# Kernel optimization log

Hardware: AMD Instinct MI355X
Metric: run time of the kernel (lower is better)

The kernel has to match this reference:

```python
import jax, jax.numpy as jnp
import numpy as np

NUM_USERS = 1_000_000
NUM_ITEMS = 1_000_000
NUM_UFEAT = 100_000
NUM_IFEAT = 100_000
DIM = 64
BATCH = 16384
T_U = 327_680   # total flat user-feature tokens (~20/sample)
T_I = 819_200   # total flat item-feature tokens (~50/sample)


def setup_inputs() -> dict:
    key = jax.random.key(0)
    ks = jax.random.split(key, 12)
    inp = {
        "user_ids": jax.random.randint(ks[0], (BATCH,), 0, NUM_USERS),
        "item_ids": jax.random.randint(ks[1], (BATCH,), 0, NUM_ITEMS),
        "user_feat_idx": jax.random.randint(ks[2], (T_U,), 0, NUM_UFEAT),
        "user_feat_val": jax.random.uniform(ks[3], (T_U,), dtype=jnp.float32),
        "user_seg": jnp.sort(jax.random.randint(ks[4], (T_U,), 0, BATCH)),
        "item_feat_idx": jax.random.randint(ks[5], (T_I,), 0, NUM_IFEAT),
        "item_feat_val": jax.random.uniform(ks[6], (T_I,), dtype=jnp.float32),
        "item_seg": jnp.sort(jax.random.randint(ks[7], (T_I,), 0, BATCH)),
        # parameters (xavier-normal-style scale)
        "user_emb": jax.random.normal(ks[8], (NUM_USERS, DIM), jnp.float32) * 0.02,
        "item_emb": jax.random.normal(ks[9], (NUM_ITEMS, DIM), jnp.float32) * 0.02,
        "user_feat_emb": jax.random.normal(ks[10], (NUM_UFEAT, DIM), jnp.float32) * 0.02,
        "item_feat_emb": jax.random.normal(ks[11], (NUM_IFEAT, DIM), jnp.float32) * 0.02,
        "user_bias": jnp.zeros((NUM_USERS,), jnp.float32),
        "item_bias": jnp.zeros((NUM_ITEMS,), jnp.float32),
        "global_bias": jnp.zeros((), jnp.float32),
    }
    return inp


def _ragged_weighted_sum(table, idx, val, seg):
    # gather rows [T, D], weight, segment-reduce to [BATCH, D]
    rows = table[idx] * val[:, None]
    return jax.ops.segment_sum(rows, seg, num_segments=BATCH)


def reference(user_ids, item_ids, user_feat_idx, user_feat_val, user_seg,
              item_feat_idx, item_feat_val, item_seg,
              user_emb, item_emb, user_feat_emb, item_feat_emb,
              user_bias, item_bias, global_bias):
    u_feat = _ragged_weighted_sum(user_feat_emb, user_feat_idx, user_feat_val, user_seg)
    i_feat = _ragged_weighted_sum(item_feat_emb, item_feat_idx, item_feat_val, item_seg)
    u = user_emb[user_ids] + u_feat          # [B, D]
    v = item_emb[item_ids] + i_feat          # [B, D]
    pred = jnp.sum(u * v, axis=1)
    pred = pred + user_bias[user_ids] + item_bias[item_ids] + global_bias
    return pred
```

## Files before the change

### kernel.cpp

```cpp
#include <hip/hip_runtime.h>

#define DIM 64

static __device__ __forceinline__ int lower_bound(const int* __restrict__ a, int n, int v) {
    int lo = 0, hi = n;
    while (lo < hi) {
        int m = (lo + hi) >> 1;
        if (a[m] < v) lo = m + 1; else hi = m;
    }
    return lo;
}

__global__ __launch_bounds__(256) void mf_fwd_kernel(
    const int* __restrict__ user_ids, const int* __restrict__ item_ids,
    const int* __restrict__ u_idx, const float* __restrict__ u_val,
    const int* __restrict__ u_seg,
    const int* __restrict__ i_idx, const float* __restrict__ i_val,
    const int* __restrict__ i_seg,
    const float* __restrict__ user_emb, const float* __restrict__ item_emb,
    const float* __restrict__ ufeat_emb, const float* __restrict__ ifeat_emb,
    const float* __restrict__ user_bias, const float* __restrict__ item_bias,
    const float* __restrict__ global_bias,
    float* __restrict__ out,
    int batch, int Tu, int Ti)
{
    const int lane = threadIdx.x & 63;
    const int wave = threadIdx.x >> 6;
    const int b = (blockIdx.x << 2) + wave;
    if (b >= batch) return;

    int us  = __builtin_amdgcn_readfirstlane(lower_bound(u_seg, Tu, b));
    int ue  = __builtin_amdgcn_readfirstlane(lower_bound(u_seg, Tu, b + 1));
    int is0 = __builtin_amdgcn_readfirstlane(lower_bound(i_seg, Ti, b));
    int ie  = __builtin_amdgcn_readfirstlane(lower_bound(i_seg, Ti, b + 1));

    const int uid = user_ids[b];
    const int iid = item_ids[b];

    float u = user_emb[(size_t)uid * DIM + lane];
    for (int t = us; t < ue; ++t) {
        int   r = u_idx[t];
        float w = u_val[t];
        u = fmaf(ufeat_emb[(size_t)r * DIM + lane], w, u);
    }

    float v = item_emb[(size_t)iid * DIM + lane];
    for (int t = is0; t < ie; ++t) {
        int   r = i_idx[t];
        float w = i_val[t];
        v = fmaf(ifeat_emb[(size_t)r * DIM + lane], w, v);
    }

    float p = u * v;
    #pragma unroll
    for (int off = 32; off > 0; off >>= 1)
        p += __shfl_xor(p, off, 64);

    if (lane == 0)
        out[b] = p + user_bias[uid] + item_bias[iid] + global_bias[0];
}

extern "C" void kernel_launch(void* const* d_in, const int* in_sizes, int n_in,
                              void* d_out, int out_size, void* d_ws, size_t ws_size,
                              hipStream_t stream) {
    const int*   user_ids    = (const int*)d_in[0];
    const int*   item_ids    = (const int*)d_in[1];
    const int*   u_idx       = (const int*)d_in[2];
    const float* u_val       = (const float*)d_in[3];
    const int*   u_seg       = (const int*)d_in[4];
    const int*   i_idx       = (const int*)d_in[5];
    const float* i_val       = (const float*)d_in[6];
    const int*   i_seg       = (const int*)d_in[7];
    const float* user_emb    = (const float*)d_in[8];
    const float* item_emb    = (const float*)d_in[9];
    const float* ufeat_emb   = (const float*)d_in[10];
    const float* ifeat_emb   = (const float*)d_in[11];
    const float* user_bias   = (const float*)d_in[12];
    const float* item_bias   = (const float*)d_in[13];
    const float* global_bias = (const float*)d_in[14];
    float* out = (float*)d_out;

    const int batch = in_sizes[0];
    const int Tu    = in_sizes[2];
    const int Ti    = in_sizes[5];

    const int blocks = (batch + 3) / 4;
    mf_fwd_kernel<<<blocks, 256, 0, stream>>>(
        user_ids, item_ids, u_idx, u_val, u_seg, i_idx, i_val, i_seg,
        user_emb, item_emb, ufeat_emb, ifeat_emb, user_bias, item_bias,
        global_bias, out, batch, Tu, Ti);
}
```

Measured before the change: 574.0 us.

## Split wave into four token groups with float4 row loads and unrolled gathers

Each 64-lane wave is split into four 16-lane groups. Each group reads a full 64-float row with float4 loads and handles every fourth token, with the token loop unrolled by eight so many independent gathers are in flight. Partial sums are combined across groups with xor shuffles, and the dot product is reduced within 16 lanes. This targets the latency-bound serial per-token gather loop, at the cost of extra masked loads on the tail iterations and more shuffle work.

```diff
diff --git a/kernel.cpp b/kernel.cpp
--- a/kernel.cpp
+++ b/kernel.cpp
@@ -1,6 +1,7 @@
 #include <hip/hip_runtime.h>
 
 #define DIM 64
+#define UNR 8
 
 static __device__ __forceinline__ int lower_bound(const int* __restrict__ a, int n, int v) {
     int lo = 0, hi = n;
@@ -9,6 +10,43 @@
         if (a[m] < v) lo = m + 1; else hi = m;
     }
     return lo;
+}
+
+static __device__ __forceinline__ float4 ragged_accum4(
+    const float* __restrict__ table,
+    const int* __restrict__ idx, const float* __restrict__ val,
+    int ts, int te, int g, int l)
+{
+    float4 acc = {0.f, 0.f, 0.f, 0.f};
+    const int n = te - ts;
+    if (n <= 0) return acc;
+    const int iters = (n + 4 * UNR - 1) / (4 * UNR);
+    for (int it = 0; it < iters; ++it) {
+        const int base = ts + it * 4 * UNR + g;
+        #pragma unroll
+        for (int j = 0; j < UNR; ++j) {
+            int tt  = base + 4 * j;
+            int ttc = min(tt, te - 1);
+            int   r = idx[ttc];
+            float w = (tt < te) ? val[ttc] : 0.0f;
+            const float4 row = *(const float4*)(table + (size_t)r * DIM + 4 * l);
+            acc.x = fmaf(row.x, w, acc.x);
+            acc.y = fmaf(row.y, w, acc.y);
+            acc.z = fmaf(row.z, w, acc.z);
+            acc.w = fmaf(row.w, w, acc.w);
+        }
+    }
+    return acc;
+}
+
+static __device__ __forceinline__ void group_reduce4(float4& a) {
+    #pragma unroll
+    for (int off = 16; off < 64; off <<= 1) {
+        a.x += __shfl_xor(a.x, off, 64);
+        a.y += __shfl_xor(a.y, off, 64);
+        a.z += __shfl_xor(a.z, off, 64);
+        a.w += __shfl_xor(a.w, off, 64);
+    }
 }
 
 __global__ __launch_bounds__(256) void mf_fwd_kernel(
@@ -26,6 +64,8 @@
 {
     const int lane = threadIdx.x & 63;
     const int wave = threadIdx.x >> 6;
+    const int g = lane >> 4;
+    const int l = lane & 15;
     const int b = (blockIdx.x << 2) + wave;
     if (b >= batch) return;
 
@@ -37,23 +77,21 @@
     const int uid = user_ids[b];
     const int iid = item_ids[b];
 
-    float u = user_emb[(size_t)uid * DIM + lane];
-    for (int t = us; t < ue; ++t) {
-        int   r = u_idx[t];
-        float w = u_val[t];
-        u = fmaf(ufeat_emb[(size_t)r * DIM + lane], w, u);
-    }
+    const float4 u0 = *(const float4*)(user_emb + (size_t)uid * DIM + 4 * l);
+    const float4 v0 = *(const float4*)(item_emb + (size_t)iid * DIM + 4 * l);
 
-    float v = item_emb[(size_t)iid * DIM + lane];
-    for (int t = is0; t < ie; ++t) {
-        int   r = i_idx[t];
-        float w = i_val[t];
-        v = fmaf(ifeat_emb[(size_t)r * DIM + lane], w, v);
-    }
+    float4 ua = ragged_accum4(ufeat_emb, u_idx, u_val, us,  ue, g, l);
+    float4 va = ragged_accum4(ifeat_emb, i_idx, i_val, is0, ie, g, l);
 
-    float p = u * v;
+    group_reduce4(ua);
+    group_reduce4(va);
+
+    const float ux = ua.x + u0.x, uy = ua.y + u0.y, uz = ua.z + u0.z, uw = ua.w + u0.w;
+    const float vx = va.x + v0.x, vy = va.y + v0.y, vz = va.z + v0.z, vw = va.w + v0.w;
+
+    float p = ux * vx + uy * vy + uz * vz + uw * vw;
     #pragma unroll
-    for (int off = 32; off > 0; off >>= 1)
+    for (int off = 1; off < 16; off <<= 1)
         p += __shfl_xor(p, off, 64);
 
     if (lane == 0)
```

Result: faster. 546.1 us (-4.9%).

## Precompute segment offsets and batch-prefetch feature rows in ragged gather

Applied to the files above, without the earlier changes.

Two small pre-kernels turn the sorted segment arrays into CSR offsets, so each wave no longer runs four binary searches over hundreds of thousands of entries. The ragged weighted sum now loads 16 indices and weights at once, issues 16 independent row gathers, and prefetches the next batch of indices while it accumulates. This exposes memory-level parallelism in place of a serial chain of dependent loads. In exchange it adds two kernel launches, a workspace write, and higher register pressure from the 16-wide buffers.

```diff
diff --git a/kernel.cpp b/kernel.cpp
--- a/kernel.cpp
+++ b/kernel.cpp
@@ -1,55 +1,94 @@
 #include <hip/hip_runtime.h>
 
 #define DIM 64
+#define NB 16
 
-static __device__ __forceinline__ int lower_bound(const int* __restrict__ a, int n, int v) {
-    int lo = 0, hi = n;
-    while (lo < hi) {
-        int m = (lo + hi) >> 1;
-        if (a[m] < v) lo = m + 1; else hi = m;
+__global__ __launch_bounds__(256) void build_offsets_kernel(
+    const int* __restrict__ seg, int T, int B, int* __restrict__ off)
+{
+    int t = blockIdx.x * blockDim.x + threadIdx.x;
+    if (t > T) return;
+    int cur  = (t == T) ? B : seg[t];
+    int prev = (t == 0) ? -1 : seg[t - 1];
+    for (int b = prev + 1; b <= cur; ++b) off[b] = t;
+}
+
+static __device__ __forceinline__ float ragged_pipelined(
+    const float* __restrict__ table, const int* __restrict__ idx,
+    const float* __restrict__ val, int ts, int te, int lane)
+{
+    float acc = 0.f;
+    const int n = te - ts;
+    if (n <= 0) return acc;
+    const int iters = (n + NB - 1) / NB;
+
+    int r[NB]; float w[NB];
+    #pragma unroll
+    for (int j = 0; j < NB; ++j) {
+        int tt = ts + j, tc = min(tt, te - 1);
+        r[j] = idx[tc];
+        w[j] = (tt < te) ? val[tc] : 0.f;
     }
-    return lo;
+
+    for (int it = 0; it < iters; ++it) {
+        float row[NB];
+        #pragma unroll
+        for (int j = 0; j < NB; ++j)
+            row[j] = table[(size_t)r[j] * DIM + lane];
+
+        const bool more = (it + 1 < iters);
+        const int nb = ts + (it + 1) * NB;
+        int r2[NB]; float w2[NB];
+        if (more) {
+            #pragma unroll
+            for (int j = 0; j < NB; ++j) {
+                int tt = nb + j, tc = min(tt, te - 1);
+                r2[j] = idx[tc];
+                w2[j] = (tt < te) ? val[tc] : 0.f;
+            }
+        }
+
+        #pragma unroll
+        for (int j = 0; j < NB; ++j)
+            acc = fmaf(row[j], w[j], acc);
+
+        if (more) {
+            #pragma unroll
+            for (int j = 0; j < NB; ++j) { r[j] = r2[j]; w[j] = w2[j]; }
+        }
+    }
+    return acc;
 }
 
 __global__ __launch_bounds__(256) void mf_fwd_kernel(
     const int* __restrict__ user_ids, const int* __restrict__ item_ids,
     const int* __restrict__ u_idx, const float* __restrict__ u_val,
-    const int* __restrict__ u_seg,
     const int* __restrict__ i_idx, const float* __restrict__ i_val,
-    const int* __restrict__ i_seg,
+    const int* __restrict__ u_off, const int* __restrict__ i_off,
     const float* __restrict__ user_emb, const float* __restrict__ item_emb,
     const float* __restrict__ ufeat_emb, const float* __restrict__ ifeat_emb,
     const float* __restrict__ user_bias, const float* __restrict__ item_bias,
     const float* __restrict__ global_bias,
-    float* __restrict__ out,
-    int batch, int Tu, int Ti)
+    float* __restrict__ out, int batch)
 {
     const int lane = threadIdx.x & 63;
     const int wave = threadIdx.x >> 6;
     const int b = (blockIdx.x << 2) + wave;
     if (b >= batch) return;
 
-    int us  = __builtin_amdgcn_readfirstlane(lower_bound(u_seg, Tu, b));
-    int ue  = __builtin_amdgcn_readfirstlane(lower_bound(u_seg, Tu, b + 1));
-    int is0 = __builtin_amdgcn_readfirstlane(lower_bound(i_seg, Ti, b));
-    int ie  = __builtin_amdgcn_readfirstlane(lower_bound(i_seg, Ti, b + 1));
+    const int us  = __builtin_amdgcn_readfirstlane(u_off[b]);
+    const int ue  = __builtin_amdgcn_readfirstlane(u_off[b + 1]);
+    const int is0 = __builtin_amdgcn_readfirstlane(i_off[b]);
+    const int ie  = __builtin_amdgcn_readfirstlane(i_off[b + 1]);
 
     const int uid = user_ids[b];
     const int iid = item_ids[b];
 
-    float u = user_emb[(size_t)uid * DIM + lane];
-    for (int t = us; t < ue; ++t) {
-        int   r = u_idx[t];
-        float w = u_val[t];
-        u = fmaf(ufeat_emb[(size_t)r * DIM + lane], w, u);
-    }
+    const float u0 = user_emb[(size_t)uid * DIM + lane];
+    const float v0 = item_emb[(size_t)iid * DIM + lane];
 
-    float v = item_emb[(size_t)iid * DIM + lane];
-    for (int t = is0; t < ie; ++t) {
-        int   r = i_idx[t];
-        float w = i_val[t];
-        v = fmaf(ifeat_emb[(size_t)r * DIM + lane], w, v);
-    }
+    const float u = u0 + ragged_pipelined(ufeat_emb, u_idx, u_val, us,  ue, lane);
+    const float v = v0 + ragged_pipelined(ifeat_emb, i_idx, i_val, is0, ie, lane);
 
     float p = u * v;
     #pragma unroll
@@ -84,9 +123,15 @@
     const int Tu    = in_sizes[2];
     const int Ti    = in_sizes[5];
 
+    int* u_off = (int*)d_ws;
+    int* i_off = u_off + (batch + 1);
+
+    build_offsets_kernel<<<(Tu + 256) / 256 + 1, 256, 0, stream>>>(u_seg, Tu, batch, u_off);
+    build_offsets_kernel<<<(Ti + 256) / 256 + 1, 256, 0, stream>>>(i_seg, Ti, batch, i_off);
+
     const int blocks = (batch + 3) / 4;
     mf_fwd_kernel<<<blocks, 256, 0, stream>>>(
-        user_ids, item_ids, u_idx, u_val, u_seg, i_idx, i_val, i_seg,
+        user_ids, item_ids, u_idx, u_val, i_idx, i_val, u_off, i_off,
         user_emb, item_emb, ufeat_emb, ifeat_emb, user_bias, item_bias,
-        global_bias, out, batch, Tu, Ti);
+        global_bias, out, batch);
 }
```

After: 485.6 us. -15.4%, faster.
